# Optimization experiments

Measured on AMD Instinct MI355X. Metric: run time of the kernel, lower is better.

The kernel has to match this reference:

```python
import jax, jax.numpy as jnp
import numpy as np

B, IN, OUT = 8192, 1024, 1024


def setup_inputs() -> dict:
    key = jax.random.key(0)
    k1, k2 = jax.random.split(key)
    x = jax.random.normal(k1, (B, IN), dtype=jnp.float32)
    W_seed = jax.random.normal(k2, (IN, OUT), dtype=jnp.float32) / np.sqrt(IN).astype(np.float32)
    b_seed = jnp.zeros((OUT,), dtype=jnp.float32)
    W_sig = jnp.zeros((2,), dtype=jnp.float32)  # mixture logits over ['dense','Toeplitz']
    b_sig = jnp.zeros((2,), dtype=jnp.float32)  # mixture logits over ['dense','None']
    A_sig = jnp.zeros((2,), dtype=jnp.float32)  # mixture logits over ['linear','relu']
    return {"x": x, "W_seed": W_seed, "b_seed": b_seed,
            "W_sig": W_sig, "b_sig": b_sig, "A_sig": A_sig}


def _toeplitz_from_seed(W_seed):
    # seed_vec = [W_seed[0, out-1], ..., W_seed[0, 1], W_seed[0,0], ..., W_seed[in-1,0]]
    in_sz, out_sz = W_seed.shape
    seed_vec = jnp.concatenate([W_seed[0, -1:0:-1], W_seed[:, 0]])  # [out-1 + in]
    # W_toep[i, j] = seed_vec[i - j + out - 1]
    idx = jnp.arange(in_sz)[:, None] - jnp.arange(out_sz)[None, :] + (out_sz - 1)
    return seed_vec[idx]  # [in, out]


def reference(x, W_seed, b_seed, W_sig, b_sig, A_sig):
    W_toep = _toeplitz_from_seed(W_seed)
    w_s = jax.nn.softmax(W_sig)
    W_core = w_s[0] * W_seed + w_s[1] * W_toep          # softmax-weighted weight mixture
    b_s = jax.nn.softmax(b_sig)
    b_core = b_s[0] * b_seed                             # 'None' branch contributes zeros
    out = x @ W_core + b_core                            # [B, out]
    a_s = jax.nn.softmax(A_sig)
    return a_s[0] * out + a_s[1] * jax.nn.relu(out)      # activation mixture
```

## Files before the change

kernel.cpp:

```cpp
#include <hip/hip_runtime.h>

typedef unsigned short ushort_t;
typedef __bf16 bf16x8 __attribute__((ext_vector_type(8)));
typedef float f32x4 __attribute__((ext_vector_type(4)));

#define AS1 __attribute__((address_space(1)))
#define AS3 __attribute__((address_space(3)))

__device__ __forceinline__ ushort_t f2bf(float f) {
    unsigned u = __builtin_bit_cast(unsigned, f);
    u = (u + 0x7fffu + ((u >> 16) & 1u)) >> 16;
    return (ushort_t)u;
}

__device__ __forceinline__ void async16(void* lds, const void* g) {
    __builtin_amdgcn_global_load_lds((const AS1 unsigned int*)g,
                                     (AS3 unsigned int*)lds, 16, 0, 0);
}

__device__ __forceinline__ void softmax2(const float* __restrict__ sig, float& s0, float& s1) {
    float a = sig[0], b = sig[1];
    float m = fmaxf(a, b);
    float e0 = __expf(a - m), e1 = __expf(b - m);
    float inv = 1.0f / (e0 + e1);
    s0 = e0 * inv; s1 = e1 * inv;
}

__device__ __forceinline__ float toep_val(const float* __restrict__ Wseed, int k, int o) {
    return (k >= o) ? Wseed[(size_t)(k - o) << 10] : Wseed[o - k];
}

__global__ __launch_bounds__(256) void prep_kernel(const float* __restrict__ x,
                                                   const float* __restrict__ Wseed,
                                                   const float* __restrict__ Wsig,
                                                   ushort_t* __restrict__ xb,
                                                   ushort_t* __restrict__ Wt) {
    int b = blockIdx.x;
    if (b < 4096) {
        int i = b * 256 + threadIdx.x;
        const float4* xp = (const float4*)x + (size_t)i * 2;
        float4 a = xp[0], c = xp[1];
        uint4 r;
        r.x = (unsigned)f2bf(a.x) | ((unsigned)f2bf(a.y) << 16);
        r.y = (unsigned)f2bf(a.z) | ((unsigned)f2bf(a.w) << 16);
        r.z = (unsigned)f2bf(c.x) | ((unsigned)f2bf(c.y) << 16);
        r.w = (unsigned)f2bf(c.z) | ((unsigned)f2bf(c.w) << 16);
        ((uint4*)xb)[i] = r;
        return;
    }
    __shared__ float T[64][65];
    int bb = b - 4096;
    int k0 = (bb >> 4) * 64;
    int o0 = (bb & 15) * 64;
    int t = threadIdx.x;
    #pragma unroll
    for (int i = 0; i < 4; ++i) {
        int lin = t + i * 256;
        int kr = lin >> 4;
        int c4 = lin & 15;
        float4 v = *(const float4*)&Wseed[(size_t)(k0 + kr) * 1024 + o0 + c4 * 4];
        T[kr][c4 * 4 + 0] = v.x;
        T[kr][c4 * 4 + 1] = v.y;
        T[kr][c4 * 4 + 2] = v.z;
        T[kr][c4 * 4 + 3] = v.w;
    }
    __syncthreads();
    float s0, s1; softmax2(Wsig, s0, s1);
    #pragma unroll
    for (int i = 0; i < 2; ++i) {
        int lin = t + i * 256;
        int oo = lin >> 3;
        int kq = (lin & 7) * 8;
        unsigned r[4];
        #pragma unroll
        for (int q = 0; q < 4; ++q) {
            float v0 = s0 * T[kq + 2 * q + 0][oo] + s1 * toep_val(Wseed, k0 + kq + 2 * q + 0, o0 + oo);
            float v1 = s0 * T[kq + 2 * q + 1][oo] + s1 * toep_val(Wseed, k0 + kq + 2 * q + 1, o0 + oo);
            r[q] = (unsigned)f2bf(v0) | ((unsigned)f2bf(v1) << 16);
        }
        *(uint4*)&Wt[(size_t)(o0 + oo) * 1024 + k0 + kq] = make_uint4(r[0], r[1], r[2], r[3]);
    }
}

#define NKT 16

__global__ __launch_bounds__(512, 2) void gemm_kernel(const ushort_t* __restrict__ Xb,
                                                      const ushort_t* __restrict__ Wt,
                                                      const float* __restrict__ bseed,
                                                      const float* __restrict__ bsig,
                                                      const float* __restrict__ asig,
                                                      float* __restrict__ out) {
    __shared__ ushort_t lds[49152];
    ushort_t* const A0v = lds;
    ushort_t* const B0v = lds + 16384;
    ushort_t* const A1v = lds + 24576;
    ushort_t* const B1v = lds + 40960;

    const int t = threadIdx.x;
    const int wv = t >> 6;
    const int lane = t & 63;

    const int orig = blockIdx.x;
    const int g = orig & 7;
    const int within = orig >> 3;
    const int rb = g * 4 + (within >> 3);
    const int cb = within & 7;
    const int brow = rb * 256;
    const int bcol = cb * 128;

    const int r0 = t >> 3;
    const int kcs = 8 * ((t & 7) ^ (r0 & 7));
    const ushort_t* gA = Xb + (size_t)(brow + r0) * 1024 + kcs;
    const ushort_t* gB = Wt + (size_t)(bcol + r0) * 1024 + kcs;

    const int wr = (wv >> 1) * 64;
    const int wcn = (wv & 1) * 64;
    const int fr = lane & 15;
    const int kg = (lane >> 4) * 8;
    const int frx = (fr & 7) << 3;

    f32x4 acc[4][4];
    #pragma unroll
    for (int i = 0; i < 4; ++i)
        #pragma unroll
        for (int j = 0; j < 4; ++j) acc[i][j] = (f32x4){0.f, 0.f, 0.f, 0.f};
    bf16x8 bfr[4][2];

    float bs0, bs1, as0, as1;
    softmax2(bsig, bs0, bs1);
    softmax2(asig, as0, as1);
    float bias[4];
    #pragma unroll
    for (int ni = 0; ni < 4; ++ni)
        bias[ni] = bs0 * bseed[bcol + wcn + ni * 16 + fr];
    asm volatile("" :: "v"(bias[0]), "v"(bias[1]), "v"(bias[2]), "v"(bias[3]),
                       "v"(as0), "v"(as1));
    asm volatile("" ::: "memory");

#define PHASE(p, Abuf, Bbuf, STAGEBLOCK)                                           \
    do {                                                                           \
        const int arow_ = wr + (p) * 16 + fr;                                      \
        bf16x8 a0 = *(const bf16x8*)&(Abuf)[arow_ * 64 + ((0 + kg) ^ frx)];        \
        bf16x8 a1 = *(const bf16x8*)&(Abuf)[arow_ * 64 + ((32 + kg) ^ frx)];       \
        if ((p) == 0) {                                                            \
            _Pragma("unroll")                                                      \
            for (int ni = 0; ni < 4; ++ni) {                                       \
                int brow_ = wcn + ni * 16 + fr;                                    \
                bfr[ni][0] = *(const bf16x8*)&(Bbuf)[brow_ * 64 + ((0 + kg) ^ frx)];  \
                bfr[ni][1] = *(const bf16x8*)&(Bbuf)[brow_ * 64 + ((32 + kg) ^ frx)]; \
            }                                                                      \
        }                                                                          \
        STAGEBLOCK                                                                 \
        asm volatile("" ::: "memory");                                             \
        __builtin_amdgcn_s_barrier();                                              \
        __builtin_amdgcn_s_setprio(1);                                             \
        _Pragma("unroll")                                                          \
        for (int ni = 0; ni < 4; ++ni) {                                           \
            acc[p][ni] = __builtin_amdgcn_mfma_f32_16x16x32_bf16(a0, bfr[ni][0],   \
                                                                 acc[p][ni], 0, 0, 0); \
            acc[p][ni] = __builtin_amdgcn_mfma_f32_16x16x32_bf16(a1, bfr[ni][1],   \
                                                                 acc[p][ni], 0, 0, 0); \
        }                                                                          \
        __builtin_amdgcn_s_setprio(0);                                             \
        asm volatile("" ::: "memory");                                             \
    } while (0)

#define KTILE(Acur, Bcur, Aoth, Both, kt1, DOSTAGE)                                \
    do {                                                                           \
        PHASE(0, Acur, Bcur, {                                                     \
            if (DOSTAGE) {                                                         \
                async16((Aoth) + wv * 512,        gA + (size_t)(kt1) * 64);        \
                async16((Aoth) + 4096 + wv * 512, gA + 65536 + (size_t)(kt1) * 64);\
            }                                                                      \
        });                                                                        \
        __builtin_amdgcn_s_barrier();                                              \
        PHASE(1, Acur, Bcur, {                                                     \
            if (DOSTAGE) {                                                         \
                async16((Aoth) + 8192 + wv * 512,  gA + 131072 + (size_t)(kt1) * 64); \
                async16((Aoth) + 12288 + wv * 512, gA + 196608 + (size_t)(kt1) * 64); \
            }                                                                      \
        });                                                                        \
        __builtin_amdgcn_s_barrier();                                              \
        PHASE(2, Acur, Bcur, {                                                     \
            if (DOSTAGE) {                                                         \
                async16((Both) + wv * 512,        gB + (size_t)(kt1) * 64);        \
                async16((Both) + 4096 + wv * 512, gB + 65536 + (size_t)(kt1) * 64);\
            }                                                                      \
        });                                                                        \
        __builtin_amdgcn_s_barrier();                                              \
        PHASE(3, Acur, Bcur, {});                                                  \
        asm volatile("s_waitcnt vmcnt(0)" ::: "memory");                           \
        __builtin_amdgcn_s_barrier();                                              \
    } while (0)

    async16(A0v + wv * 512,          gA);
    async16(A0v + 4096 + wv * 512,   gA + 65536);
    async16(A0v + 8192 + wv * 512,   gA + 131072);
    async16(A0v + 12288 + wv * 512,  gA + 196608);
    async16(B0v + wv * 512,          gB);
    async16(B0v + 4096 + wv * 512,   gB + 65536);
    asm volatile("s_waitcnt vmcnt(0)" ::: "memory");
    __builtin_amdgcn_s_barrier();

    for (int kt = 0; kt < 14; kt += 2) {
        KTILE(A0v, B0v, A1v, B1v, kt + 1, true);
        KTILE(A1v, B1v, A0v, B0v, kt + 2, true);
    }
    KTILE(A0v, B0v, A1v, B1v, 15, true);
    KTILE(A1v, B1v, A0v, B0v, 0, false);

    #pragma unroll
    for (int ni = 0; ni < 4; ++ni) {
        int col = bcol + wcn + ni * 16 + fr;
        #pragma unroll
        for (int mi = 0; mi < 4; ++mi) {
            int row = brow + wr + mi * 16 + (lane >> 4) * 4;
            #pragma unroll
            for (int r = 0; r < 4; ++r) {
                float v = acc[mi][ni][r] + bias[ni];
                out[(size_t)(row + r) * 1024 + col] = as0 * v + as1 * fmaxf(v, 0.f);
            }
        }
    }
#undef PHASE
#undef KTILE
}

__global__ __launch_bounds__(256) void naive_kernel(const float* __restrict__ x,
                                                    const float* __restrict__ Wseed,
                                                    const float* __restrict__ bseed,
                                                    const float* __restrict__ Wsig,
                                                    const float* __restrict__ bsig,
                                                    const float* __restrict__ asig,
                                                    float* __restrict__ out) {
    int idx = blockIdx.x * 256 + threadIdx.x;
    int b = idx >> 10, o = idx & 1023;
    float ws0, ws1, bs0, bs1, as0, as1;
    softmax2(Wsig, ws0, ws1);
    softmax2(bsig, bs0, bs1);
    softmax2(asig, as0, as1);
    float s = 0.f;
    const float* xr = x + (size_t)b * 1024;
    for (int k = 0; k < 1024; ++k) {
        float wc = ws0 * Wseed[((size_t)k << 10) + o] + ws1 * toep_val(Wseed, k, o);
        s += xr[k] * wc;
    }
    float v = s + bs0 * bseed[o];
    out[idx] = as0 * v + as1 * fmaxf(v, 0.f);
}

extern "C" void kernel_launch(void* const* d_in, const int* in_sizes, int n_in,
                              void* d_out, int out_size, void* d_ws, size_t ws_size,
                              hipStream_t stream) {
    const float* x     = (const float*)d_in[0];
    const float* Wseed = (const float*)d_in[1];
    const float* bseed = (const float*)d_in[2];
    const float* Wsig  = (const float*)d_in[3];
    const float* bsig  = (const float*)d_in[4];
    const float* Asig  = (const float*)d_in[5];
    float* out = (float*)d_out;

    const size_t need = (2u << 20) + (16u << 20) + 1024;
    if (ws_size < need) {
        naive_kernel<<<dim3(8192 * 1024 / 256), dim3(256), 0, stream>>>(
            x, Wseed, bseed, Wsig, bsig, Asig, out);
        return;
    }

    ushort_t* Wt = (ushort_t*)d_ws;
    ushort_t* Xb = (ushort_t*)((char*)d_ws + (2u << 20));

    prep_kernel<<<dim3(4096 + 256), dim3(256), 0, stream>>>(x, Wseed, Wsig, Xb, Wt);
    gemm_kernel<<<dim3(256), dim3(512), 0, stream>>>(Xb, Wt, bseed, bsig, Asig, out);
}
```

Before: 42.98 us.

## Switch GEMM LDS pipeline from double to triple buffering

Replaces the double-buffered LDS staging with a three-buffer ring. Loads now run two k-tiles ahead, and the wait becomes a partial vmcnt(6) instead of draining all loads each tile. The goal is to hide global-load latency better behind the MFMA work. In exchange, LDS use per block grows from 96KB to 144KB. With launch_bounds(512,2) that likely exceeds the per-CU LDS budget, which could cut occupancy to one block per CU.

```diff
diff --git a/kernel.cpp b/kernel.cpp
--- a/kernel.cpp
+++ b/kernel.cpp
@@ -90,11 +90,10 @@
                                                       const float* __restrict__ bsig,
                                                       const float* __restrict__ asig,
                                                       float* __restrict__ out) {
-    __shared__ ushort_t lds[49152];
-    ushort_t* const A0v = lds;
-    ushort_t* const B0v = lds + 16384;
-    ushort_t* const A1v = lds + 24576;
-    ushort_t* const B1v = lds + 40960;
+    __shared__ ushort_t lds[73728];
+    ushort_t* p0 = lds;
+    ushort_t* p1 = lds + 24576;
+    ushort_t* p2 = lds + 49152;
 
     const int t = threadIdx.x;
     const int wv = t >> 6;
@@ -137,20 +136,20 @@
                        "v"(as0), "v"(as1));
     asm volatile("" ::: "memory");
 
-#define PHASE(p, Abuf, Bbuf, STAGEBLOCK)                                           \
+#define PH(p, STAGEBLK)                                                            \
     do {                                                                           \
         const int arow_ = wr + (p) * 16 + fr;                                      \
-        bf16x8 a0 = *(const bf16x8*)&(Abuf)[arow_ * 64 + ((0 + kg) ^ frx)];        \
-        bf16x8 a1 = *(const bf16x8*)&(Abuf)[arow_ * 64 + ((32 + kg) ^ frx)];       \
+        bf16x8 a0 = *(const bf16x8*)&p0[arow_ * 64 + ((0 + kg) ^ frx)];            \
+        bf16x8 a1 = *(const bf16x8*)&p0[arow_ * 64 + ((32 + kg) ^ frx)];           \
         if ((p) == 0) {                                                            \
             _Pragma("unroll")                                                      \
             for (int ni = 0; ni < 4; ++ni) {                                       \
-                int brow_ = wcn + ni * 16 + fr;                                    \
-                bfr[ni][0] = *(const bf16x8*)&(Bbuf)[brow_ * 64 + ((0 + kg) ^ frx)];  \
-                bfr[ni][1] = *(const bf16x8*)&(Bbuf)[brow_ * 64 + ((32 + kg) ^ frx)]; \
+                int br_ = wcn + ni * 16 + fr;                                      \
+                bfr[ni][0] = *(const bf16x8*)&p0[16384 + br_ * 64 + ((0 + kg) ^ frx)];  \
+                bfr[ni][1] = *(const bf16x8*)&p0[16384 + br_ * 64 + ((32 + kg) ^ frx)]; \
             }                                                                      \
         }                                                                          \
-        STAGEBLOCK                                                                 \
+        STAGEBLK                                                                   \
         asm volatile("" ::: "memory");                                             \
         __builtin_amdgcn_s_barrier();                                              \
         __builtin_amdgcn_s_setprio(1);                                             \
@@ -162,52 +161,41 @@
                                                                  acc[p][ni], 0, 0, 0); \
         }                                                                          \
         __builtin_amdgcn_s_setprio(0);                                             \
-        asm volatile("" ::: "memory");                                             \
     } while (0)
 
-#define KTILE(Acur, Bcur, Aoth, Both, kt1, DOSTAGE)                                \
-    do {                                                                           \
-        PHASE(0, Acur, Bcur, {                                                     \
-            if (DOSTAGE) {                                                         \
-                async16((Aoth) + wv * 512,        gA + (size_t)(kt1) * 64);        \
-                async16((Aoth) + 4096 + wv * 512, gA + 65536 + (size_t)(kt1) * 64);\
-            }                                                                      \
-        });                                                                        \
-        __builtin_amdgcn_s_barrier();                                              \
-        PHASE(1, Acur, Bcur, {                                                     \
-            if (DOSTAGE) {                                                         \
-                async16((Aoth) + 8192 + wv * 512,  gA + 131072 + (size_t)(kt1) * 64); \
-                async16((Aoth) + 12288 + wv * 512, gA + 196608 + (size_t)(kt1) * 64); \
-            }                                                                      \
-        });                                                                        \
-        __builtin_amdgcn_s_barrier();                                              \
-        PHASE(2, Acur, Bcur, {                                                     \
-            if (DOSTAGE) {                                                         \
-                async16((Both) + wv * 512,        gB + (size_t)(kt1) * 64);        \
-                async16((Both) + 4096 + wv * 512, gB + 65536 + (size_t)(kt1) * 64);\
-            }                                                                      \
-        });                                                                        \
-        __builtin_amdgcn_s_barrier();                                              \
-        PHASE(3, Acur, Bcur, {});                                                  \
-        asm volatile("s_waitcnt vmcnt(0)" ::: "memory");                           \
-        __builtin_amdgcn_s_barrier();                                              \
-    } while (0)
-
-    async16(A0v + wv * 512,          gA);
-    async16(A0v + 4096 + wv * 512,   gA + 65536);
-    async16(A0v + 8192 + wv * 512,   gA + 131072);
-    async16(A0v + 12288 + wv * 512,  gA + 196608);
-    async16(B0v + wv * 512,          gB);
-    async16(B0v + 4096 + wv * 512,   gB + 65536);
-    asm volatile("s_waitcnt vmcnt(0)" ::: "memory");
+    async16(p0 + wv * 512,          gA);
+    async16(p0 + 4096 + wv * 512,   gA + 65536);
+    async16(p0 + 8192 + wv * 512,   gA + 131072);
+    async16(p0 + 12288 + wv * 512,  gA + 196608);
+    async16(p0 + 16384 + wv * 512,  gB);
+    async16(p0 + 20480 + wv * 512,  gB + 65536);
+    async16(p1 + wv * 512,          gA + 64);
+    async16(p1 + 4096 + wv * 512,   gA + 65536 + 64);
+    async16(p1 + 8192 + wv * 512,   gA + 131072 + 64);
+    async16(p1 + 12288 + wv * 512,  gA + 196608 + 64);
+    async16(p1 + 16384 + wv * 512,  gB + 64);
+    async16(p1 + 20480 + wv * 512,  gB + 65536 + 64);
+    asm volatile("s_waitcnt vmcnt(6)" ::: "memory");
     __builtin_amdgcn_s_barrier();
 
-    for (int kt = 0; kt < 14; kt += 2) {
-        KTILE(A0v, B0v, A1v, B1v, kt + 1, true);
-        KTILE(A1v, B1v, A0v, B0v, kt + 2, true);
-    }
-    KTILE(A0v, B0v, A1v, B1v, 15, true);
-    KTILE(A1v, B1v, A0v, B0v, 0, false);
+    for (int T = 0; T < NKT; ++T) {
+        const size_t t2 = (size_t)(T + 2) * 64;
+        const bool dost = (T < NKT - 2);
+        PH(0, { if (dost) { async16(p2 + wv * 512,          gA + t2);
+                            async16(p2 + 4096 + wv * 512,   gA + 65536 + t2); } });
+        __builtin_amdgcn_s_barrier();
+        PH(1, { if (dost) { async16(p2 + 8192 + wv * 512,   gA + 131072 + t2);
+                            async16(p2 + 12288 + wv * 512,  gA + 196608 + t2); } });
+        __builtin_amdgcn_s_barrier();
+        PH(2, { if (dost) { async16(p2 + 16384 + wv * 512,  gB + t2);
+                            async16(p2 + 20480 + wv * 512,  gB + 65536 + t2); } });
+        __builtin_amdgcn_s_barrier();
+        PH(3, {});
+        if (T < NKT - 2)        { asm volatile("s_waitcnt vmcnt(6)" ::: "memory"); }
+        else if (T == NKT - 2)  { asm volatile("s_waitcnt vmcnt(0)" ::: "memory"); }
+        __builtin_amdgcn_s_barrier();
+        ushort_t* tmp_ = p0; p0 = p1; p1 = p2; p2 = tmp_;
+    }
 
     #pragma unroll
     for (int ni = 0; ni < 4; ++ni) {
@@ -222,8 +210,7 @@
             }
         }
     }
-#undef PHASE
-#undef KTILE
+#undef PH
 }
 
 __global__ __launch_bounds__(256) void naive_kernel(const float* __restrict__ x,
```

Result: slower. 44.38 us (+3.3%).
